# Kernel tuning notes

Hardware: AMD Instinct MI355X
Metric: run time of the kernel (lower is better)

## Reference

```python
import jax, jax.numpy as jnp
import numpy as np

B, CIN, COUT, RES, K, WDIM = 16, 512, 512, 64, 3, 512


def setup_inputs() -> dict:
    key = jax.random.key(0)
    ks = jax.random.split(key, 6)
    return {
        "x": jax.random.normal(ks[0], (B, CIN, RES, RES), jnp.float32),
        "w": jax.random.normal(ks[1], (B, WDIM), jnp.float32),
        "affine_w": jax.random.normal(ks[2], (3 * CIN, WDIM), jnp.float32),
        "affine_b": jnp.ones((3 * CIN,), jnp.float32),  # bias_init=1
        "weight": jax.random.normal(ks[3], (COUT, CIN, K, K), jnp.float32),
        "bias": jnp.zeros((COUT,), jnp.float32),
        "noise_const": jax.random.normal(ks[4], (RES, RES), jnp.float32),
        "noise_strength": jnp.zeros((), jnp.float32),
    }


def reference(x, w, affine_w, affine_b, weight, bias, noise_const, noise_strength):
    b, cin, h, wd = x.shape
    cout, _, kh, kw = weight.shape
    wdim = affine_w.shape[1]
    # StyleSplit: FullyConnectedLayer (weight_gain = 1/sqrt(w_dim)) -> chunk3 -> m1*m2+m3
    proj = w @ (affine_w * (1.0 / np.sqrt(wdim))).T + affine_b  # [B, 3*Cin]
    m1, m2, m3 = jnp.split(proj, 3, axis=1)
    styles = m1 * m2 + m3  # [B, Cin]
    # modulate + demodulate (fused_modconv path)
    ww = weight[None] * styles[:, None, :, None, None]  # [B, Cout, Cin, kh, kw]
    dcoefs = jax.lax.rsqrt(jnp.sum(ww * ww, axis=(2, 3, 4)) + 1e-8)  # [B, Cout]
    ww = ww * dcoefs[:, :, None, None, None]
    # batch-as-groups conv (flip_weight=True -> plain cross-correlation), padding = k//2
    pad = kh // 2
    xg = x.reshape(1, b * cin, h, wd)
    wg = ww.reshape(b * cout, cin, kh, kw)
    y = jax.lax.conv_general_dilated(
        xg, wg, window_strides=(1, 1), padding=((pad, pad), (pad, pad)),
        dimension_numbers=("NCHW", "OIHW", "NCHW"), feature_group_count=b)
    y = y.reshape(b, cout, h, wd)
    # const noise
    y = y + noise_const * noise_strength
    # bias_act: lrelu(slope 0.2) with def_gain sqrt(2), gain=1, no clamp
    y = jax.nn.leaky_relu(y + bias[None, :, None, None], 0.2) * np.sqrt(2.0).astype(np.float32)
    return y
```

## Files before the change

### kernel.cpp

```cpp
#include <hip/hip_runtime.h>


#define NCI  512
#define NCO  512

typedef __attribute__((ext_vector_type(8))) short short8;
typedef __attribute__((ext_vector_type(4))) float f32x4;

#define GLDS16(g, l) __builtin_amdgcn_global_load_lds( \
    (const __attribute__((address_space(1))) void*)(g), \
    (__attribute__((address_space(3))) void*)(l), 16, 0, 0)

static __device__ __forceinline__ unsigned short f2bf(float f) {
  unsigned int u = __float_as_uint(f);
  u += 0x7fffu + ((u >> 16) & 1u);
  return (unsigned short)(u >> 16);
}

__global__ __launch_bounds__(256) void k_styles(
    const float* __restrict__ w, const float* __restrict__ aw,
    const float* __restrict__ ab, float* __restrict__ styles) {
  const int ci0 = blockIdx.x * 32, b = blockIdx.y;
  __shared__ float ws[512];
  __shared__ float pm[3][32];
  const int t = threadIdx.x;
  ws[t] = w[b * 512 + t];
  ws[t + 256] = w[b * 512 + 256 + t];
  __syncthreads();
  const int r = t >> 3, k = t & 7;
#pragma unroll
  for (int pass = 0; pass < 3; ++pass) {
    const float* row = aw + (size_t)(ci0 + r + pass * 512) * 512;
    float a = 0.f;
#pragma unroll 4
    for (int i = 0; i < 16; ++i) {
      float4 v = *(const float4*)(row + i * 32 + k * 4);
      float4 u = *(const float4*)(&ws[i * 32 + k * 4]);
      a += v.x * u.x + v.y * u.y + v.z * u.z + v.w * u.w;
    }
    a += __shfl_xor(a, 1); a += __shfl_xor(a, 2); a += __shfl_xor(a, 4);
    if (k == 0) pm[pass][r] = a;
  }
  __syncthreads();
  if (t < 32) {
    const float g = 0.04419417382415922f;
    int j = ci0 + t;
    float m1 = pm[0][t] * g + ab[j];
    float m2 = pm[1][t] * g + ab[j + 512];
    float m3 = pm[2][t] * g + ab[j + 1024];
    styles[b * 512 + j] = m1 * m2 + m3;
  }
}

__global__ __launch_bounds__(256) void k_wt(
    const float* __restrict__ wgt, short* __restrict__ wb2, float* __restrict__ wsq) {
  const int co_blk = blockIdx.x & 7, ci_blk = blockIdx.x >> 3;
  __shared__ short wtile[18432];
  const int t = threadIdx.x;
#pragma unroll
  for (int i = 0; i < 8; ++i) {
    int idx = i * 256 + t;
    int co_l = idx >> 5, ci_l = idx & 31;
    int co = co_blk * 64 + co_l, ci = ci_blk * 32 + ci_l;
    const float* p = wgt + ((size_t)co * 512 + ci) * 9;
    int base = (co_l >> 4) * 512 + (((ci_l >> 3) & 3) * 16 + (co_l & 15)) * 8 + (ci_l & 7);
    float s = 0.f;
#pragma unroll
    for (int kk = 0; kk < 9; ++kk) {
      float v = p[kk];
      s += v * v;
      wtile[kk * 2048 + base] = (short)f2bf(v);
    }
    wsq[(size_t)co * 512 + ci] = s;
  }
  __syncthreads();
  short8* dst = (short8*)(wb2 + (size_t)(ci_blk * 8 + co_blk) * 18432);
  const short8* src = (const short8*)wtile;
#pragma unroll
  for (int j = 0; j < 9; ++j) dst[j * 256 + t] = src[j * 256 + t];
}

__global__ __launch_bounds__(256) void k_dcoef(
    const float* __restrict__ wsq, const float* __restrict__ styles,
    float* __restrict__ dcoef) {
  const int co0 = blockIdx.x * 32, b = blockIdx.y;
  __shared__ float ss[512];
  const int t = threadIdx.x;
  float s0 = styles[b * 512 + t], s1 = styles[b * 512 + 256 + t];
  ss[t] = s0 * s0;
  ss[t + 256] = s1 * s1;
  __syncthreads();
  const int r = t >> 3, k = t & 7;
  const float* row = wsq + (size_t)(co0 + r) * 512;
  float a = 0.f;
#pragma unroll 4
  for (int i = 0; i < 16; ++i) {
    float4 v = *(const float4*)(row + i * 32 + k * 4);
    float4 u = *(const float4*)(&ss[i * 32 + k * 4]);
    a += v.x * u.x + v.y * u.y + v.z * u.z + v.w * u.w;
  }
  a += __shfl_xor(a, 1); a += __shfl_xor(a, 2); a += __shfl_xor(a, 4);
  if (k == 0) dcoef[b * 512 + co0 + r] = 1.0f / sqrtf(a + 1e-8f);
}

__global__ __launch_bounds__(256) void k_xt(
    const float* __restrict__ x, const float* __restrict__ styles,
    short* __restrict__ xt) {
  const int px0 = blockIdx.x * 64, ci0 = blockIdx.y * 32, b = blockIdx.z;
  __shared__ float tile[32][68];
  const int t = threadIdx.x;
  {
    const int cil = t >> 4, pxq = t & 15;
#pragma unroll
    for (int half = 0; half < 2; ++half) {
      const int c = cil + half * 16;
      float4 v = *(const float4*)(x + ((size_t)(b * 512 + ci0 + c)) * 4096 + px0 + pxq * 4);
      float sc = styles[b * 512 + ci0 + c];
      v.x *= sc; v.y *= sc; v.z *= sc; v.w *= sc;
      *(float4*)(&tile[c][4 * (pxq ^ (c & 15))]) = v;
    }
  }
  __syncthreads();
  {
    const int pxl = t >> 2, cig = t & 3;
    short8 o;
#pragma unroll
    for (int e = 0; e < 8; ++e) {
      int R = cig * 8 + e;
      o[e] = (short)f2bf(tile[R][4 * ((pxl >> 2) ^ (R & 15)) + (pxl & 3)]);
    }
    *(short8*)(xt + ((size_t)(b * 4096 + px0 + pxl)) * 512 + ci0 + cig * 8) = o;
  }
}

__global__ __launch_bounds__(256, 2) void k_conv(
    const short* __restrict__ xt, const short* __restrict__ wb2,
    const float* __restrict__ dcoef, const float* __restrict__ bias,
    const float* __restrict__ noise, const float* __restrict__ nstr,
    float* __restrict__ out) {
  const int bid = blockIdx.x;
  const int logical = (bid & 7) * 128 + (bid >> 3);
  const int coi  = logical & 7;
  const int pair = logical >> 3;
  const int b    = pair >> 3;
  const int h0   = (pair & 7) * 8;
  const int co0  = coi * 64;

  __shared__ short xs[10][4][66][8];
  __shared__ short wls[9][4][64][8];
  const int t = threadIdx.x;
  const int lane = t & 63, wave = t >> 6;
  const int lrow = lane & 15, lq = lane >> 4;

  const short8 z8 = {0, 0, 0, 0, 0, 0, 0, 0};
  if (t < 80) {
    int r = t / 8, pc = t & 7;
    *(short8*)(&xs[r][pc >> 1][(pc & 1) ? 65 : 0][0]) = z8;
  }
  if (h0 == 0) {
    for (int i2 = t; i2 < 264; i2 += 256) ((short8*)&xs[0][0][0][0])[i2] = z8;
  }
  if (h0 == 56) {
    for (int i2 = t; i2 < 264; i2 += 256) ((short8*)&xs[9][0][0][0])[i2] = z8;
  }

  f32x4 acc[4][8];
#pragma unroll
  for (int m = 0; m < 4; ++m)
#pragma unroll
    for (int n = 0; n < 8; ++n)
#pragma unroll
      for (int e = 0; e < 4; ++e) acc[m][n][e] = 0.f;

  const size_t xb = (size_t)b * 4096 * 512;

  for (int cb = 0; cb < 16; ++cb) {
    const int ci0 = cb * 32;
#pragma unroll
    for (int i2 = 0; i2 < 10; ++i2) {
      int rp = i2 * 4 + wave;
      int r = rp >> 2, p = rp & 3;
      int row = h0 - 1 + r;
      if ((unsigned)row < 64u) {
        const short* g = xt + xb + ((size_t)(row * 64 + lane)) * 512 + ci0 + p * 8;
        GLDS16(g, &xs[r][p][1][0]);
      }
    }
    const short* wbase = wb2 + (size_t)(cb * 8 + coi) * 18432;
#pragma unroll
    for (int i2 = 0; i2 < 9; ++i2) {
      int c = i2 * 4 + wave;
      GLDS16(wbase + c * 512 + lane * 8, ((short*)wls) + c * 512);
    }
    __syncthreads();

#pragma unroll
    for (int kw = 0; kw < 3; ++kw) {
      short8 bx[4][4];
#pragma unroll
      for (int r = 0; r < 4; ++r)
#pragma unroll
        for (int c = 0; c < 4; ++c)
          bx[r][c] = *(const short8*)(&xs[2 * wave + r][lq][c * 16 + lrow + kw][0]);
#pragma unroll
      for (int kh = 0; kh < 3; ++kh) {
        const int kk = kh * 3 + kw;
        short8 af[4];
#pragma unroll
        for (int m = 0; m < 4; ++m)
          af[m] = *(const short8*)(&wls[kk][m][lane][0]);
#pragma unroll
        for (int m = 0; m < 4; ++m)
#pragma unroll
          for (int n = 0; n < 8; ++n)
            acc[m][n] = __builtin_amdgcn_mfma_f32_16x16x32_bf16(
                af[m], bx[kh + (n >> 2)][n & 3], acc[m][n], 0, 0, 0);
      }
    }
    __syncthreads();
  }

  const float ns = nstr[0];
  float dc[4][4], bv[4][4];
#pragma unroll
  for (int m = 0; m < 4; ++m)
#pragma unroll
    for (int r = 0; r < 4; ++r) {
      int co = co0 + m * 16 + lq * 4 + r;
      dc[m][r] = dcoef[b * NCO + co];
      bv[m][r] = bias[co];
    }
#pragma unroll
  for (int n = 0; n < 8; ++n) {
    int h = h0 + 2 * wave + (n >> 2);
    int wcol = (n & 3) * 16 + lrow;
    float nz = noise[h * 64 + wcol] * ns;
#pragma unroll
    for (int m = 0; m < 4; ++m) {
#pragma unroll
      for (int r = 0; r < 4; ++r) {
        int co = co0 + m * 16 + lq * 4 + r;
        float v = acc[m][n][r] * dc[m][r] + nz + bv[m][r];
        v = (v > 0.f ? v : 0.2f * v) * 1.4142135623730951f;
        out[(((size_t)b * NCO + co) * 64 + h) * 64 + wcol] = v;
      }
    }
  }
}

extern "C" void kernel_launch(void* const* d_in, const int* in_sizes, int n_in,
                              void* d_out, int out_size, void* d_ws, size_t ws_size,
                              hipStream_t stream) {
  const float* x    = (const float*)d_in[0];
  const float* w    = (const float*)d_in[1];
  const float* aw   = (const float*)d_in[2];
  const float* ab   = (const float*)d_in[3];
  const float* wgt  = (const float*)d_in[4];
  const float* bias = (const float*)d_in[5];
  const float* nc   = (const float*)d_in[6];
  const float* ns   = (const float*)d_in[7];
  float* out = (float*)d_out;

  char* ws = (char*)d_ws;
  float* styles = (float*)(ws);
  float* dcoef  = (float*)(ws + 32768);
  float* wsq    = (float*)(ws + 65536);
  short* wb2    = (short*)(ws + 1114112);
  short* xt     = (short*)(ws + 5832704);

  k_styles<<<dim3(16, 16), dim3(256), 0, stream>>>(w, aw, ab, styles);
  k_wt<<<dim3(128), dim3(256), 0, stream>>>(wgt, wb2, wsq);
  k_dcoef<<<dim3(16, 16), dim3(256), 0, stream>>>(wsq, styles, dcoef);
  k_xt<<<dim3(64, 16, 16), dim3(256), 0, stream>>>(x, styles, xt);
  k_conv<<<dim3(1024), dim3(256), 0, stream>>>(xt, wb2, dcoef, bias, nc, ns, out);
}
```

Baseline: 487.3 us.

## Double-buffer conv LDS tiles and loop channel chunks inside transpose kernel

The conv kernel now keeps two LDS buffers for the input and weight tiles and issues the global-to-LDS loads for the next channel block while MFMAs run on the current one. This removes the exposed load latency per channel step. LDS use doubles, so launch bounds drop to one block per CU and occupancy falls. Separately, the transpose kernel now loops over all 16 channel chunks per block instead of launching a block per chunk, giving a smaller grid with more work per block.

```diff
diff --git a/kernel.cpp b/kernel.cpp
--- a/kernel.cpp
+++ b/kernel.cpp
@@ -106,11 +106,13 @@
 __global__ __launch_bounds__(256) void k_xt(
     const float* __restrict__ x, const float* __restrict__ styles,
     short* __restrict__ xt) {
-  const int px0 = blockIdx.x * 64, ci0 = blockIdx.y * 32, b = blockIdx.z;
+  const int px0 = blockIdx.x * 64, b = blockIdx.y;
   __shared__ float tile[32][68];
   const int t = threadIdx.x;
-  {
-    const int cil = t >> 4, pxq = t & 15;
+  const int cil = t >> 4, pxq = t & 15;
+  const int pxl = t >> 2, cig = t & 3;
+  for (int cc = 0; cc < 16; ++cc) {
+    const int ci0 = cc * 32;
 #pragma unroll
     for (int half = 0; half < 2; ++half) {
       const int c = cil + half * 16;
@@ -119,21 +121,21 @@
       v.x *= sc; v.y *= sc; v.z *= sc; v.w *= sc;
       *(float4*)(&tile[c][4 * (pxq ^ (c & 15))]) = v;
     }
-  }
-  __syncthreads();
-  {
-    const int pxl = t >> 2, cig = t & 3;
-    short8 o;
-#pragma unroll
-    for (int e = 0; e < 8; ++e) {
-      int R = cig * 8 + e;
-      o[e] = (short)f2bf(tile[R][4 * ((pxl >> 2) ^ (R & 15)) + (pxl & 3)]);
-    }
-    *(short8*)(xt + ((size_t)(b * 4096 + px0 + pxl)) * 512 + ci0 + cig * 8) = o;
-  }
-}
-
-__global__ __launch_bounds__(256, 2) void k_conv(
+    __syncthreads();
+    {
+      short8 o;
+#pragma unroll
+      for (int e = 0; e < 8; ++e) {
+        int R = cig * 8 + e;
+        o[e] = (short)f2bf(tile[R][4 * ((pxl >> 2) ^ (R & 15)) + (pxl & 3)]);
+      }
+      *(short8*)(xt + ((size_t)(b * 4096 + px0 + pxl)) * 512 + ci0 + cig * 8) = o;
+    }
+    __syncthreads();
+  }
+}
+
+__global__ __launch_bounds__(256, 1) void k_conv(
     const short* __restrict__ xt, const short* __restrict__ wb2,
     const float* __restrict__ dcoef, const float* __restrict__ bias,
     const float* __restrict__ noise, const float* __restrict__ nstr,
@@ -146,22 +148,24 @@
   const int h0   = (pair & 7) * 8;
   const int co0  = coi * 64;
 
-  __shared__ short xs[10][4][66][8];
-  __shared__ short wls[9][4][64][8];
+  __shared__ short xs[2][10][4][66][8];
+  __shared__ short wls[2][9][4][64][8];
   const int t = threadIdx.x;
   const int lane = t & 63, wave = t >> 6;
   const int lrow = lane & 15, lq = lane >> 4;
 
   const short8 z8 = {0, 0, 0, 0, 0, 0, 0, 0};
-  if (t < 80) {
-    int r = t / 8, pc = t & 7;
-    *(short8*)(&xs[r][pc >> 1][(pc & 1) ? 65 : 0][0]) = z8;
+  for (int i2 = t; i2 < 160; i2 += 256) {
+    int nb = i2 / 80, j = i2 % 80, r = j / 8, pc = j & 7;
+    *(short8*)(&xs[nb][r][pc >> 1][(pc & 1) ? 65 : 0][0]) = z8;
   }
   if (h0 == 0) {
-    for (int i2 = t; i2 < 264; i2 += 256) ((short8*)&xs[0][0][0][0])[i2] = z8;
+    for (int i2 = t; i2 < 528; i2 += 256)
+      ((short8*)&xs[i2 / 264][0][0][0][0])[i2 % 264] = z8;
   }
   if (h0 == 56) {
-    for (int i2 = t; i2 < 264; i2 += 256) ((short8*)&xs[9][0][0][0])[i2] = z8;
+    for (int i2 = t; i2 < 528; i2 += 256)
+      ((short8*)&xs[i2 / 264][9][0][0][0])[i2 % 264] = z8;
   }
 
   f32x4 acc[4][8];
@@ -174,25 +178,31 @@
 
   const size_t xb = (size_t)b * 4096 * 512;
 
-  for (int cb = 0; cb < 16; ++cb) {
+  auto stage = [&](int nb, int cb) {
     const int ci0 = cb * 32;
 #pragma unroll
     for (int i2 = 0; i2 < 10; ++i2) {
-      int rp = i2 * 4 + wave;
-      int r = rp >> 2, p = rp & 3;
+      int r = i2, p = wave;
       int row = h0 - 1 + r;
       if ((unsigned)row < 64u) {
         const short* g = xt + xb + ((size_t)(row * 64 + lane)) * 512 + ci0 + p * 8;
-        GLDS16(g, &xs[r][p][1][0]);
+        GLDS16(g, &xs[nb][r][p][1][0]);
       }
     }
     const short* wbase = wb2 + (size_t)(cb * 8 + coi) * 18432;
 #pragma unroll
     for (int i2 = 0; i2 < 9; ++i2) {
       int c = i2 * 4 + wave;
-      GLDS16(wbase + c * 512 + lane * 8, ((short*)wls) + c * 512);
-    }
-    __syncthreads();
+      GLDS16(wbase + c * 512 + lane * 8, ((short*)&wls[nb][0][0][0][0]) + c * 512);
+    }
+  };
+
+  stage(0, 0);
+  __syncthreads();
+
+  int cur = 0;
+  for (int cb = 0; cb < 16; ++cb) {
+    if (cb < 15) stage(cur ^ 1, cb + 1);
 
 #pragma unroll
     for (int kw = 0; kw < 3; ++kw) {
@@ -201,14 +211,14 @@
       for (int r = 0; r < 4; ++r)
 #pragma unroll
         for (int c = 0; c < 4; ++c)
-          bx[r][c] = *(const short8*)(&xs[2 * wave + r][lq][c * 16 + lrow + kw][0]);
+          bx[r][c] = *(const short8*)(&xs[cur][2 * wave + r][lq][c * 16 + lrow + kw][0]);
 #pragma unroll
       for (int kh = 0; kh < 3; ++kh) {
         const int kk = kh * 3 + kw;
         short8 af[4];
 #pragma unroll
         for (int m = 0; m < 4; ++m)
-          af[m] = *(const short8*)(&wls[kk][m][lane][0]);
+          af[m] = *(const short8*)(&wls[cur][kk][m][lane][0]);
 #pragma unroll
         for (int m = 0; m < 4; ++m)
 #pragma unroll
@@ -218,6 +228,7 @@
       }
     }
     __syncthreads();
+    cur ^= 1;
   }
 
   const float ns = nstr[0];
@@ -271,6 +282,6 @@
   k_styles<<<dim3(16, 16), dim3(256), 0, stream>>>(w, aw, ab, styles);
   k_wt<<<dim3(128), dim3(256), 0, stream>>>(wgt, wb2, wsq);
   k_dcoef<<<dim3(16, 16), dim3(256), 0, stream>>>(wsq, styles, dcoef);
-  k_xt<<<dim3(64, 16, 16), dim3(256), 0, stream>>>(x, styles, xt);
+  k_xt<<<dim3(64, 16), dim3(256), 0, stream>>>(x, styles, xt);
   k_conv<<<dim3(1024), dim3(256), 0, stream>>>(xt, wb2, dcoef, bias, nc, ns, out);
 }
```

New measurement: 571.4 us. 17.3% more time.
